# Kernel tuning notes

Measured on AMD Instinct MI355X. Metric: run time of the kernel, lower is better.

Reference implementation:

```python
import jax, jax.numpy as jnp
import numpy as np

B, C, H, W, R = 32, 512, 32, 32, 64  # batch, in_channels, spatial, rd_channels
EPS = 1e-5


def setup_inputs() -> dict:
    key = jax.random.key(0)
    ks = jax.random.split(key, 12)
    s_in = 1.0 / np.sqrt(C)
    s_rd = 1.0 / np.sqrt(R)
    return {
        "x": jax.random.normal(ks[0], (B, C, H, W), dtype=jnp.float32),
        "Wt": jax.random.normal(ks[1], (R, C), dtype=jnp.float32) * s_in,
        "bt": jax.random.normal(ks[2], (R,), dtype=jnp.float32) * 0.01,
        "Wp": jax.random.normal(ks[3], (R, C), dtype=jnp.float32) * s_in,
        "bp": jax.random.normal(ks[4], (R,), dtype=jnp.float32) * 0.01,
        "Wg": jax.random.normal(ks[5], (R, C), dtype=jnp.float32) * s_in,
        "bg": jax.random.normal(ks[6], (R,), dtype=jnp.float32) * 0.01,
        "Wz": jax.random.normal(ks[7], (C, R), dtype=jnp.float32) * s_rd,
        "bz": jax.random.normal(ks[8], (C,), dtype=jnp.float32) * 0.01,
        "gamma": jax.random.normal(ks[9], (C,), dtype=jnp.float32) * 0.1 + 1.0,
        "beta": jax.random.normal(ks[10], (C,), dtype=jnp.float32) * 0.1,
        "bn_mean": jnp.zeros((C,), dtype=jnp.float32),
        "bn_var": jnp.ones((C,), dtype=jnp.float32),
    }


def reference(x, Wt, bt, Wp, bp, Wg, bg, Wz, bz, gamma, beta, bn_mean, bn_var):
    scale = C ** (-0.5)  # note: uses in_channels, as in the source
    Bn, _, Hh, Ww = x.shape
    N = Hh * Ww
    xf = x.reshape(Bn, C, N)                       # [B, C, N]
    # 1x1 convs == per-position linear projections
    t = jnp.einsum('bcn,rc->bnr', xf, Wt) + bt           # [B, N, R]
    p = jnp.einsum('bcn,rc->brn', xf, Wp) + bp[:, None]  # [B, R, N]
    g = jnp.einsum('bcn,rc->bnr', xf, Wg) + bg           # [B, N, R]
    att = jnp.einsum('bnr,brm->bnm', t, p) * scale       # [B, N, N]
    att = jax.nn.softmax(att, axis=2)
    y = jnp.einsum('bnm,bmr->bnr', att, g)               # [B, N, R]
    z = jnp.einsum('bnr,cr->bcn', y, Wz) + bz[:, None]   # [B, C, N]
    # BatchNorm2d (inference mode)
    zn = (z - bn_mean[:, None]) * jax.lax.rsqrt(bn_var[:, None] + EPS)
    zn = zn * gamma[:, None] + beta[:, None]
    return zn.reshape(Bn, C, Hh, Ww) + x
```

## Files before the change

### kernel.cpp

```cpp
#include <hip/hip_runtime.h>

namespace {

constexpr int B = 32;
constexpr int C = 512;
constexpr int N = 1024;
constexpr int R = 64;
constexpr float SCALE = 0.044194173824159216f;
constexpr float EPS = 1e-5f;

typedef float f32x4 __attribute__((ext_vector_type(4)));
typedef short bf16x8 __attribute__((ext_vector_type(8)));

__device__ __forceinline__ unsigned short f2b(float f) {
  union { unsigned int i; float f; } x;
  x.f = f;
  unsigned int v = x.i;
  return (unsigned short)((v + 0x7fffu + ((v >> 16) & 1u)) >> 16);
}

__device__ __forceinline__ int xadr(int row, int ku16) {
  return (row * 272 + ku16 * 2) ^ (((row >> 3) & 7) << 4);
}

__global__ __launch_bounds__(256) void k_prep(
    const float* __restrict__ Wt, const float* __restrict__ Wp,
    const float* __restrict__ Wg, const float* __restrict__ Wz,
    unsigned short* __restrict__ wtf, unsigned short* __restrict__ wpf,
    unsigned short* __restrict__ wgf, unsigned short* __restrict__ wzf)
{
  int i = blockIdx.x * 256 + (int)threadIdx.x;
  int m = i >> 12, o = i & 4095;
  const float* src;
  unsigned short* dst;
  int sidx;
  if (m < 3) {
    int rt = o >> 10, kk = (o >> 6) & 15, l = o & 63;
    int r = rt * 16 + (l & 15), c = kk * 32 + (l >> 4) * 8;
    sidx = r * 512 + c;
    src = (m == 0) ? Wt : (m == 1) ? Wp : Wg;
    dst = (m == 0) ? wtf : (m == 1) ? wpf : wgf;
  } else {
    int ct = o >> 7, kk = (o >> 6) & 1, l = o & 63;
    int row = ct * 16 + (l & 15), k = kk * 32 + (l >> 4) * 8;
    sidx = row * 64 + k;
    src = Wz;
    dst = wzf;
  }
  float4 a = *(const float4*)(src + sidx);
  float4 bb = *(const float4*)(src + sidx + 4);
  ushort4 lo, hi;
  lo.x = f2b(a.x); lo.y = f2b(a.y); lo.z = f2b(a.z); lo.w = f2b(a.w);
  hi.x = f2b(bb.x); hi.y = f2b(bb.y); hi.z = f2b(bb.z); hi.w = f2b(bb.w);
  *(ushort4*)(dst + (size_t)o * 8) = lo;
  *(ushort4*)(dst + (size_t)o * 8 + 4) = hi;
}

__global__ __launch_bounds__(256) void k1_proj(
    const float* __restrict__ x,
    const unsigned short* __restrict__ wtf, const unsigned short* __restrict__ wpf,
    const unsigned short* __restrict__ wgf,
    const float* __restrict__ bt, const float* __restrict__ bp,
    const float* __restrict__ bg,
    unsigned short* __restrict__ t_s, unsigned short* __restrict__ p_s,
    unsigned short* __restrict__ g_s)
{
  __shared__ unsigned short xs[2][64 * 136];

  const int b = blockIdx.y, n0 = blockIdx.x * 64;
  const int tid = (int)threadIdx.x, l = tid & 63, w = tid >> 6;
  const int col = l & 15, q = l >> 4;
  const int n4 = col * 4;
  const int c0a = w * 16 + q * 4;

  float4 v[2][4];
  auto issue = [&](int ch) {
    #pragma unroll
    for (int g = 0; g < 2; ++g) {
      int cb = ch * 128 + c0a + g * 64;
      #pragma unroll
      for (int i = 0; i < 4; ++i)
        v[g][i] = *(const float4*)(x + ((size_t)(b * C + cb + i) << 10) + n0 + n4);
    }
  };
  auto store = [&](int buf) {
    #pragma unroll
    for (int g = 0; g < 2; ++g) {
      int crel = c0a + g * 64;
      #pragma unroll
      for (int j = 0; j < 4; ++j) {
        unsigned int u0 = (unsigned int)f2b(((const float*)&v[g][0])[j]) |
                          ((unsigned int)f2b(((const float*)&v[g][1])[j]) << 16);
        unsigned int u1 = (unsigned int)f2b(((const float*)&v[g][2])[j]) |
                          ((unsigned int)f2b(((const float*)&v[g][3])[j]) << 16);
        uint2 val; val.x = u0; val.y = u1;
        *(uint2*)((char*)&xs[buf][0] + xadr(n4 + j, crel)) = val;
      }
    }
  };

  issue(0);
  store(0);
  __syncthreads();

  f32x4 tacc[4], pacc[4], gacc[4];
  #pragma unroll
  for (int i = 0; i < 4; ++i) {
    tacc[i] = (f32x4){0.f, 0.f, 0.f, 0.f};
    pacc[i] = (f32x4){0.f, 0.f, 0.f, 0.f};
    gacc[i] = (f32x4){0.f, 0.f, 0.f, 0.f};
  }

  int cur = 0;
  for (int ch = 0; ch < 4; ++ch) {
    if (ch < 3) issue(ch + 1);
    const char* xb = (const char*)&xs[cur][0];
    #pragma unroll
    for (int kk4 = 0; kk4 < 4; ++kk4) {
      int kkg = ch * 4 + kk4;
      bf16x8 aT = *(const bf16x8*)(xb + xadr(w * 16 + col, kk4 * 32 + q * 8));
      bf16x8 aG = *(const bf16x8*)(wgf + ((size_t)((w * 16 + kkg) * 64 + l) << 3));
      #pragma unroll
      for (int rt = 0; rt < 4; ++rt) {
        bf16x8 bT = *(const bf16x8*)(wtf + ((size_t)((rt * 16 + kkg) * 64 + l) << 3));
        tacc[rt] = __builtin_amdgcn_mfma_f32_16x16x32_bf16(aT, bT, tacc[rt], 0, 0, 0);
        bf16x8 bP = *(const bf16x8*)(wpf + ((size_t)((rt * 16 + kkg) * 64 + l) << 3));
        pacc[rt] = __builtin_amdgcn_mfma_f32_16x16x32_bf16(aT, bP, pacc[rt], 0, 0, 0);
        bf16x8 bG = *(const bf16x8*)(xb + xadr(rt * 16 + col, kk4 * 32 + q * 8));
        gacc[rt] = __builtin_amdgcn_mfma_f32_16x16x32_bf16(aG, bG, gacc[rt], 0, 0, 0);
      }
    }
    if (ch < 3) {
      __syncthreads();
      store(cur ^ 1);
      __syncthreads();
      cur ^= 1;
    }
  }

  #pragma unroll
  for (int rt = 0; rt < 4; ++rt) {
    int r = rt * 16 + col;
    float btv = bt[r], bpv = bp[r];
    #pragma unroll
    for (int reg = 0; reg < 4; ++reg) {
      int n = n0 + w * 16 + q * 4 + reg;
      size_t o = (((size_t)b << 10) + n) * 64 + r;
      t_s[o] = f2b((tacc[rt][reg] + btv) * SCALE);
      p_s[o] = f2b(pacc[rt][reg] + bpv);
    }
  }
  #pragma unroll
  for (int reg = 0; reg < 4; ++reg) {
    int r = w * 16 + q * 4 + reg;
    float bgv = bg[r];
    #pragma unroll
    for (int nt = 0; nt < 4; ++nt) {
      size_t o = (((size_t)b << 6) + r) * 1024 + n0 + nt * 16 + col;
      g_s[o] = f2b(gacc[nt][reg] + bgv);
    }
  }
}

__global__ __launch_bounds__(256) void k2_attn(
    const unsigned short* __restrict__ t_s, const unsigned short* __restrict__ p_s,
    const unsigned short* __restrict__ g_s, float* __restrict__ y_part,
    float* __restrict__ l_part)
{
  __shared__ unsigned short pl[4][16 * 72];

  const int bid = (int)blockIdx.x;
  const int br = bid & 7, nqs = (bid >> 3) & 31, bq = bid >> 8;
  const int b = bq * 8 + br;
  const int nq = nqs >> 1, split = nqs & 1;
  const int n0 = nq * 64;
  const int m0base = split * 512;

  const int tid = (int)threadIdx.x, l = tid & 63, w = tid >> 6;
  const int col = l & 15, q = l >> 4;

  bf16x8 qf[2];
  #pragma unroll
  for (int kk = 0; kk < 2; ++kk)
    qf[kk] = *(const bf16x8*)(t_s + (((size_t)b << 10) + n0 + w * 16 + col) * 64 +
                              kk * 32 + q * 8);

  f32x4 yacc[4];
  float lsum[4];
  #pragma unroll
  for (int i = 0; i < 4; ++i) {
    yacc[i] = (f32x4){0.f, 0.f, 0.f, 0.f};
    lsum[i] = 0.f;
  }

  unsigned short* plw = &pl[w][0];

  for (int mt = 0; mt < 8; ++mt) {
    const int m0 = m0base + mt * 64;

    f32x4 sacc[4];
    #pragma unroll
    for (int jt = 0; jt < 4; ++jt) {
      sacc[jt] = (f32x4){0.f, 0.f, 0.f, 0.f};
      #pragma unroll
      for (int kk = 0; kk < 2; ++kk) {
        bf16x8 pf = *(const bf16x8*)(p_s + (((size_t)b << 10) + m0 + jt * 16 + col) * 64 +
                                     kk * 32 + q * 8);
        sacc[jt] = __builtin_amdgcn_mfma_f32_16x16x32_bf16(qf[kk], pf, sacc[jt], 0, 0, 0);
      }
    }

    #pragma unroll
    for (int jt = 0; jt < 4; ++jt)
      #pragma unroll
      for (int reg = 0; reg < 4; ++reg) {
        float pv = __expf(sacc[jt][reg] - 3.0f);
        lsum[reg] += pv;
        plw[(q * 4 + reg) * 72 + jt * 16 + col] = f2b(pv);
      }

    bf16x8 paf[2];
    #pragma unroll
    for (int kj = 0; kj < 2; ++kj)
      paf[kj] = *(const bf16x8*)&plw[col * 72 + kj * 32 + q * 8];
    #pragma unroll
    for (int rt = 0; rt < 4; ++rt)
      #pragma unroll
      for (int kj = 0; kj < 2; ++kj) {
        bf16x8 gf = *(const bf16x8*)(g_s + (((size_t)b << 6) + rt * 16 + col) * 1024 +
                                     m0 + kj * 32 + q * 8);
        yacc[rt] = __builtin_amdgcn_mfma_f32_16x16x32_bf16(paf[kj], gf, yacc[rt], 0, 0, 0);
      }
  }

  const size_t ybase = ((size_t)(split * B + b) << 10);
  #pragma unroll
  for (int reg = 0; reg < 4; ++reg) {
    int n = n0 + w * 16 + q * 4 + reg;
    #pragma unroll
    for (int rt = 0; rt < 4; ++rt)
      y_part[(ybase + n) * 64 + rt * 16 + col] = yacc[rt][reg];
    float red = lsum[reg];
    red += __shfl_xor(red, 1);
    red += __shfl_xor(red, 2);
    red += __shfl_xor(red, 4);
    red += __shfl_xor(red, 8);
    if (col == 0) l_part[ybase + n] = red;
  }
}

__global__ __launch_bounds__(256) void k3_out(
    const float* __restrict__ y_part, const float* __restrict__ l_part,
    const unsigned short* __restrict__ wzf,
    const float* __restrict__ bz, const float* __restrict__ gma,
    const float* __restrict__ bet, const float* __restrict__ bmean,
    const float* __restrict__ bvar, const float* __restrict__ x,
    float* __restrict__ out)
{
  __shared__ unsigned short ys[256 * 72];

  const int c0 = blockIdx.x * 64, n0 = blockIdx.y * 256, b = blockIdx.z;
  const int tid = (int)threadIdx.x, l = tid & 63, w = tid >> 6;
  const int col = l & 15, q = l >> 4;

  const float* y0 = y_part + (((size_t)b << 10)) * 64;
  const float* y1 = y_part + (((size_t)(B + b) << 10)) * 64;
  const float* l0 = l_part + ((size_t)b << 10);
  const float* l1 = l_part + ((size_t)(B + b) << 10);

  #pragma unroll
  for (int k = 0; k < 8; ++k) {
    int idx = tid + k * 256;
    int row = idx >> 3;
    int seg = (idx & 7) * 8;
    int n = n0 + row;
    float inv = 1.f / (l0[n] + l1[n]);
    const float* a0 = y0 + (size_t)n * 64 + seg;
    const float* a1 = y1 + (size_t)n * 64 + seg;
    float4 u0 = *(const float4*)a0;
    float4 u1 = *(const float4*)(a0 + 4);
    float4 v0 = *(const float4*)a1;
    float4 v1 = *(const float4*)(a1 + 4);
    uint4 pk;
    pk.x = (unsigned int)f2b((u0.x + v0.x) * inv) |
           ((unsigned int)f2b((u0.y + v0.y) * inv) << 16);
    pk.y = (unsigned int)f2b((u0.z + v0.z) * inv) |
           ((unsigned int)f2b((u0.w + v0.w) * inv) << 16);
    pk.z = (unsigned int)f2b((u1.x + v1.x) * inv) |
           ((unsigned int)f2b((u1.y + v1.y) * inv) << 16);
    pk.w = (unsigned int)f2b((u1.z + v1.z) * inv) |
           ((unsigned int)f2b((u1.w + v1.w) * inv) << 16);
    *(uint4*)&ys[row * 72 + seg] = pk;
  }
  __syncthreads();

  const int ct = (c0 >> 4) + w;
  bf16x8 aW0 = *(const bf16x8*)(wzf + ((size_t)((ct * 2 + 0) * 64 + l) << 3));
  bf16x8 aW1 = *(const bf16x8*)(wzf + ((size_t)((ct * 2 + 1) * 64 + l) << 3));

  f32x4 acc[16];
  #pragma unroll
  for (int i = 0; i < 16; ++i) acc[i] = (f32x4){0.f, 0.f, 0.f, 0.f};

  #pragma unroll
  for (int nt = 0; nt < 16; ++nt) {
    bf16x8 b0 = *(const bf16x8*)&ys[(nt * 16 + col) * 72 + q * 8];
    acc[nt] = __builtin_amdgcn_mfma_f32_16x16x32_bf16(aW0, b0, acc[nt], 0, 0, 0);
    bf16x8 b1 = *(const bf16x8*)&ys[(nt * 16 + col) * 72 + 32 + q * 8];
    acc[nt] = __builtin_amdgcn_mfma_f32_16x16x32_bf16(aW1, b1, acc[nt], 0, 0, 0);
  }

  #pragma unroll
  for (int reg = 0; reg < 4; ++reg) {
    int c = c0 + w * 16 + q * 4 + reg;
    float s = gma[c] * rsqrtf(bvar[c] + EPS);
    float a = (bz[c] - bmean[c]) * s + bet[c];
    #pragma unroll
    for (int nt = 0; nt < 16; ++nt) {
      size_t oi = ((size_t)(b * C + c) << 10) + n0 + nt * 16 + col;
      out[oi] = acc[nt][reg] * s + a + x[oi];
    }
  }
}

}

extern "C" void kernel_launch(void* const* d_in, const int* in_sizes, int n_in,
                              void* d_out, int out_size, void* d_ws, size_t ws_size,
                              hipStream_t stream)
{
  const float* x   = (const float*)d_in[0];
  const float* Wt  = (const float*)d_in[1];
  const float* bt  = (const float*)d_in[2];
  const float* Wp  = (const float*)d_in[3];
  const float* bp  = (const float*)d_in[4];
  const float* Wg  = (const float*)d_in[5];
  const float* bg  = (const float*)d_in[6];
  const float* Wz  = (const float*)d_in[7];
  const float* bz  = (const float*)d_in[8];
  const float* gma = (const float*)d_in[9];
  const float* bet = (const float*)d_in[10];
  const float* bmn = (const float*)d_in[11];
  const float* bvr = (const float*)d_in[12];
  float* out = (float*)d_out;

  unsigned short* base = (unsigned short*)d_ws;
  unsigned short* wtf = base;
  unsigned short* wpf = base + 32768;
  unsigned short* wgf = base + 65536;
  unsigned short* wzf = base + 98304;
  unsigned short* t_s = base + 131072;
  const size_t SZ = (size_t)B * N * R;
  unsigned short* p_s = t_s + SZ;
  unsigned short* g_s = p_s + SZ;
  float* y_part = (float*)(g_s + SZ);
  float* l_part = y_part + 2 * SZ;

  k_prep<<<64, 256, 0, stream>>>(Wt, Wp, Wg, Wz, wtf, wpf, wgf, wzf);
  k1_proj<<<dim3(16, 32), 256, 0, stream>>>(x, wtf, wpf, wgf, bt, bp, bg,
                                            t_s, p_s, g_s);
  k2_attn<<<1024, 256, 0, stream>>>(t_s, p_s, g_s, y_part, l_part);
  k3_out<<<dim3(8, 4, 32), 256, 0, stream>>>(y_part, l_part, wzf, bz, gma, bet,
                                             bmn, bvr, x, out);
}
```

Measured before the change: 244.8 us.

## Stage P and G tiles through double-buffered swizzled LDS in attention kernel

After: 229.2 us. 6.4% less time.

```diff
diff --git a/kernel.cpp b/kernel.cpp
--- a/kernel.cpp
+++ b/kernel.cpp
@@ -21,6 +21,10 @@
 
 __device__ __forceinline__ int xadr(int row, int ku16) {
   return (row * 272 + ku16 * 2) ^ (((row >> 3) & 7) << 4);
+}
+
+__device__ __forceinline__ int sw128(int row, int byteInRow) {
+  return (row * 128 + byteInRow) ^ ((row & 7) << 4);
 }
 
 __global__ __launch_bounds__(256) void k_prep(
@@ -167,12 +171,14 @@
     const unsigned short* __restrict__ g_s, float* __restrict__ y_part,
     float* __restrict__ l_part)
 {
-  __shared__ unsigned short pl[4][16 * 72];
+  __shared__ unsigned short ps[2][64 * 64];
+  __shared__ unsigned short gs[2][64 * 64];
+  __shared__ unsigned short pl[4][16 * 64];
 
   const int bid = (int)blockIdx.x;
-  const int br = bid & 7, nqs = (bid >> 3) & 31, bq = bid >> 8;
+  const int br = bid & 7, s = (bid >> 3) & 31, bq = bid >> 8;
   const int b = bq * 8 + br;
-  const int nq = nqs >> 1, split = nqs & 1;
+  const int nq = s >> 1, split = s & 1;
   const int n0 = nq * 64;
   const int m0base = split * 512;
 
@@ -185,6 +191,28 @@
     qf[kk] = *(const bf16x8*)(t_s + (((size_t)b << 10) + n0 + w * 16 + col) * 64 +
                               kk * 32 + q * 8);
 
+  const int srow = tid >> 3;
+  const int ssegB = (tid & 7) * 16;
+  float4 ldp[2], ldg[2];
+  auto issue = [&](int m0) {
+    #pragma unroll
+    for (int k = 0; k < 2; ++k) {
+      int row = srow + k * 32;
+      ldp[k] = *(const float4*)((const char*)p_s +
+               ((((size_t)b << 10) + m0 + row) * 64) * 2 + ssegB);
+      ldg[k] = *(const float4*)((const char*)g_s +
+               ((((size_t)b << 6) + row) * 1024 + m0) * 2 + ssegB);
+    }
+  };
+  auto store = [&](int buf) {
+    #pragma unroll
+    for (int k = 0; k < 2; ++k) {
+      int row = srow + k * 32;
+      *(float4*)((char*)&ps[buf][0] + sw128(row, ssegB)) = ldp[k];
+      *(float4*)((char*)&gs[buf][0] + sw128(row, ssegB)) = ldg[k];
+    }
+  };
+
   f32x4 yacc[4];
   float lsum[4];
   #pragma unroll
@@ -193,10 +221,15 @@
     lsum[i] = 0.f;
   }
 
-  unsigned short* plw = &pl[w][0];
-
+  char* plw = (char*)&pl[w][0];
+
+  issue(m0base);
+  store(0);
+  __syncthreads();
+
+  int cur = 0;
   for (int mt = 0; mt < 8; ++mt) {
-    const int m0 = m0base + mt * 64;
+    if (mt < 7) issue(m0base + (mt + 1) * 64);
 
     f32x4 sacc[4];
     #pragma unroll
@@ -204,8 +237,8 @@
       sacc[jt] = (f32x4){0.f, 0.f, 0.f, 0.f};
       #pragma unroll
       for (int kk = 0; kk < 2; ++kk) {
-        bf16x8 pf = *(const bf16x8*)(p_s + (((size_t)b << 10) + m0 + jt * 16 + col) * 64 +
-                                     kk * 32 + q * 8);
+        bf16x8 pf = *(const bf16x8*)((const char*)&ps[cur][0] +
+                                     sw128(jt * 16 + col, kk * 64 + q * 16));
         sacc[jt] = __builtin_amdgcn_mfma_f32_16x16x32_bf16(qf[kk], pf, sacc[jt], 0, 0, 0);
       }
     }
@@ -216,21 +249,28 @@
       for (int reg = 0; reg < 4; ++reg) {
         float pv = __expf(sacc[jt][reg] - 3.0f);
         lsum[reg] += pv;
-        plw[(q * 4 + reg) * 72 + jt * 16 + col] = f2b(pv);
+        *(unsigned short*)(plw + sw128(q * 4 + reg, jt * 32 + col * 2)) = f2b(pv);
       }
 
     bf16x8 paf[2];
     #pragma unroll
     for (int kj = 0; kj < 2; ++kj)
-      paf[kj] = *(const bf16x8*)&plw[col * 72 + kj * 32 + q * 8];
+      paf[kj] = *(const bf16x8*)(plw + sw128(col, kj * 64 + q * 16));
     #pragma unroll
     for (int rt = 0; rt < 4; ++rt)
       #pragma unroll
       for (int kj = 0; kj < 2; ++kj) {
-        bf16x8 gf = *(const bf16x8*)(g_s + (((size_t)b << 6) + rt * 16 + col) * 1024 +
-                                     m0 + kj * 32 + q * 8);
+        bf16x8 gf = *(const bf16x8*)((const char*)&gs[cur][0] +
+                                     sw128(rt * 16 + col, kj * 64 + q * 16));
         yacc[rt] = __builtin_amdgcn_mfma_f32_16x16x32_bf16(paf[kj], gf, yacc[rt], 0, 0, 0);
       }
+
+    if (mt < 7) {
+      __syncthreads();
+      store(cur ^ 1);
+      __syncthreads();
+      cur ^= 1;
+    }
   }
 
   const size_t ybase = ((size_t)(split * B + b) << 10);
```
